# Kernel tuning notes

Hardware: AMD Instinct MI355X
Metric: run time of the kernel (lower is better)

Reference implementation:

```python
import jax, jax.numpy as jnp
import numpy as np

IN_CH, OUT_CH, K, STRIDE, PAD, NUM_POINTS = 16, 32, 3, 1, 1, 3
NUM_INPUTS = IN_CH * K * K  # 144
BATCH, H, W = 8, 32, 32


def setup_inputs() -> dict:
    key = jax.random.key(0)
    k1, k2, k3 = jax.random.split(key, 3)
    x = jax.random.normal(k1, (BATCH, IN_CH, H, W), dtype=jnp.float32)
    # sorted breakpoint positions per (input, output) pair in [-1, 1]
    base = jnp.linspace(-1.0, 1.0, NUM_POINTS, dtype=jnp.float32)
    jitter = 0.2 * (jax.random.uniform(k2, (NUM_INPUTS, OUT_CH, NUM_POINTS), dtype=jnp.float32) - 0.5) / NUM_POINTS
    positions = jnp.sort(base[None, None, :] + jitter, axis=-1)  # (I, O, P), sorted
    values = 0.1 * jax.random.normal(k3, (NUM_INPUTS, OUT_CH, NUM_POINTS), dtype=jnp.float32)
    return {"x": x, "positions": positions, "values": values}


def _gather_pt(table, idx):
    # table: (I, O, P), idx: (N, I, O) -> (N, I, O)
    return jnp.take_along_axis(table[None], idx[..., None], axis=-1)[..., 0]


def _piecewise(patches, positions, values):
    # patches: (N, I); positions/values: (I, O, P)
    P = positions.shape[-1]
    # bucket index: number of breakpoints <= x, clipped to a valid segment
    cmp = patches[:, :, None, None] >= positions[None]       # (N, I, O, P)
    idx = jnp.clip(cmp.sum(axis=-1) - 1, 0, P - 2)           # (N, I, O)
    pl = _gather_pt(positions, idx)
    pr = _gather_pt(positions, idx + 1)
    vl = _gather_pt(values, idx)
    vr = _gather_pt(values, idx + 1)
    t = (patches[:, :, None] - pl) / (pr - pl)               # (N, I, O)
    y = vl + t * (vr - vl)                                   # per-pair piecewise-linear value
    return y.sum(axis=1)                                     # (N, O): sum over input dims


def reference(x, positions, values):
    B, C, Hi, Wi = x.shape
    Ho = (Hi + 2 * PAD - K) // STRIDE + 1
    Wo = (Wi + 2 * PAD - K) // STRIDE + 1
    # im2col / unfold: (B, C*K*K, Ho, Wo) with (c, kh, kw) feature ordering like torch unfold
    patches = jax.lax.conv_general_dilated_patches(
        x, (K, K), (STRIDE, STRIDE), ((PAD, PAD), (PAD, PAD)))
    patches = patches.reshape(B, NUM_INPUTS, Ho * Wo).transpose(0, 2, 1).reshape(-1, NUM_INPUTS)
    out = _piecewise(patches, positions, values)             # (B*Ho*Wo, O)
    out = out.reshape(B, Ho * Wo, OUT_CH).transpose(0, 2, 1)
    return out.reshape(B, OUT_CH, Ho, Wo)
```

## Files before the change

### kernel.cpp

```cpp
#include <hip/hip_runtime.h>

#define IN_CH 16
#define OUT_CH 32
#define NUM_INPUTS 144
#define H_ 32
#define W_ 32

typedef __attribute__((ext_vector_type(2))) float f32x2;
typedef __attribute__((ext_vector_type(4))) float f32x4;

__global__ __launch_bounds__(512, 4) void apc_fused(
        const float* __restrict__ x,
        const float* __restrict__ pos,
        const float* __restrict__ val,
        float* __restrict__ out) {
    __shared__ f32x4 ltA[NUM_INPUTS * 16];
    __shared__ f32x2 ltD[NUM_INPUTS * 16];
    __shared__ float lx[IN_CH * 4 * 16];
    __shared__ f32x2 bpart[512];
    __shared__ f32x2 B0f[16];

    int tid  = threadIdx.x;
    int bx   = blockIdx.x;
    int b    = bx >> 6;
    int t64  = bx & 63;
    int row0 = (t64 >> 2) * 2;
    int col0 = (t64 & 3) * 8;

    #pragma unroll
    for (int it = 0; it < 2; ++it) {
        int s  = tid + it * 512;
        int c  = s >> 6;
        int rr = (s >> 4) & 3;
        int cl = s & 15;
        int gr = row0 + rr - 1;
        int gc = col0 + cl - 1;
        float v = 0.f;
        if (cl < 10 && (unsigned)gr < (unsigned)H_ && (unsigned)gc < (unsigned)W_)
            v = x[((b * IN_CH + c) * H_ + gr) * W_ + gc];
        lx[s] = v;
    }

    {
        int opb = tid & 15;
        int ib  = tid >> 4;
        f32x2 bs = {0.f, 0.f};
        #pragma unroll
        for (int k = 0; k < 5; ++k) {
            int i = ib + 32 * k;
            if (i < NUM_INPUTS) {
                const float* pp = pos + i * 96 + opb * 6;
                const float* vv = val + i * 96 + opb * 6;
                float q0a = pp[0], q1a = pp[1], q2a = pp[2];
                float q0b = pp[3], q1b = pp[4], q2b = pp[5];
                float w0a = vv[0], w1a = vv[1], w2a = vv[2];
                float w0b = vv[3], w1b = vv[4], w2b = vv[5];
                float s0a = (w1a - w0a) * __builtin_amdgcn_rcpf(q1a - q0a);
                float s1a = (w2a - w1a) * __builtin_amdgcn_rcpf(q2a - q1a);
                float s0b = (w1b - w0b) * __builtin_amdgcn_rcpf(q1b - q0b);
                float s1b = (w2b - w1b) * __builtin_amdgcn_rcpf(q2b - q1b);
                ltA[i * 16 + opb] = (f32x4){q1a, q1b, s0a, s0b};
                ltD[i * 16 + opb] = (f32x2){s1a - s0a, s1b - s0b};
                bs.x += w0a - s0a * q0a;
                bs.y += w0b - s0b * q0b;
            }
        }
        bpart[tid] = bs;
    }
    __syncthreads();

    if (tid < 16) {
        f32x2 s = {0.f, 0.f};
        #pragma unroll
        for (int g2 = 0; g2 < 32; ++g2) s += bpart[g2 * 16 + tid];
        B0f[tid] = s;
    }

    int wid  = tid >> 6;
    int lane = tid & 63;
    int sg   = lane >> 4;
    int op   = lane & 15;
    int r0   = sg >> 1;
    int cb   = (sg & 1) * 4;
    int c0   = wid * 2;

    f32x2 aacc[4], hacc[4];
    const f32x2 zz = {0.f, 0.f};
    #pragma unroll
    for (int j = 0; j < 4; ++j) { aacc[j] = zz; hacc[j] = zz; }

    const float* lxb = lx + (c0 * 4 + r0) * 16 + cb;
    const f32x4* Ab  = ltA + c0 * 144 + op;
    const f32x2* Db  = ltD + c0 * 144 + op;

    #pragma unroll
    for (int dc = 0; dc < 2; ++dc) {
        float w[3][6];
        #pragma unroll
        for (int dr = 0; dr < 3; ++dr) {
            f32x4 u = *(const f32x4*)(lxb + (dc * 4 + dr) * 16);
            f32x2 v = *(const f32x2*)(lxb + (dc * 4 + dr) * 16 + 4);
            w[dr][0] = u.x; w[dr][1] = u.y; w[dr][2] = u.z; w[dr][3] = u.w;
            w[dr][4] = v.x; w[dr][5] = v.y;
        }
        #pragma unroll
        for (int kh = 0; kh < 3; ++kh) {
            #pragma unroll
            for (int kw = 0; kw < 3; ++kw) {
                int ti = (dc * 9 + kh * 3 + kw) * 16;
                f32x4 A = Ab[ti];
                f32x2 D = Db[ti];
                f32x2 P = {A.x, A.y};
                f32x2 M = {A.z, A.w};
                #pragma unroll
                for (int j = 0; j < 4; ++j) {
                    f32x2 q = {w[kh][kw + j], w[kh][kw + j]};
                    aacc[j] = __builtin_elementwise_fma(M, q, aacc[j]);
                    hacc[j] = __builtin_elementwise_fma(
                        D, __builtin_elementwise_max(q - P, zz), hacc[j]);
                }
            }
        }
    }

    __syncthreads();
    {
        f32x2 s0 = aacc[0] + hacc[0], s1 = aacc[1] + hacc[1];
        f32x2 s2 = aacc[2] + hacc[2], s3 = aacc[3] + hacc[3];
        int rb = (wid * 64 + lane) * 2;
        ltA[rb + 0] = (f32x4){s0.x, s0.y, s1.x, s1.y};
        ltA[rb + 1] = (f32x4){s2.x, s2.y, s3.x, s3.y};
    }
    __syncthreads();

    if (tid < 256) {
        const f32x2* red = (const f32x2*)ltA;
        int opx = tid >> 4;
        int p   = tid & 15;
        int rr  = p >> 3;
        int cl  = p & 7;
        int sgx = rr * 2 + (cl >> 2);
        int j   = cl & 3;
        int base = (sgx * 16 + opx) * 4 + j;
        f32x2 s = B0f[opx];
        #pragma unroll
        for (int wv = 0; wv < 8; ++wv) s += red[wv * 256 + base];
        int oidx = ((b * OUT_CH + 2 * opx) * H_ + (row0 + rr)) * W_ + (col0 + cl);
        out[oidx]            = s.x;
        out[oidx + H_ * W_]  = s.y;
    }
}

extern "C" void kernel_launch(void* const* d_in, const int* in_sizes, int n_in,
                              void* d_out, int out_size, void* d_ws, size_t ws_size,
                              hipStream_t stream) {
    const float* x   = (const float*)d_in[0];
    const float* pos = (const float*)d_in[1];
    const float* val = (const float*)d_in[2];

    apc_fused<<<dim3(512), dim3(512), 0, stream>>>(x, pos, val, (float*)d_out);
}
```

Baseline: 63.74 us.

## Precompute piecewise-linear tables once in a separate kernel via workspace

```diff
diff --git a/kernel.cpp b/kernel.cpp
--- a/kernel.cpp
+++ b/kernel.cpp
@@ -5,19 +5,66 @@
 #define NUM_INPUTS 144
 #define H_ 32
 #define W_ 32
+#define NTAB 2304
 
 typedef __attribute__((ext_vector_type(2))) float f32x2;
 typedef __attribute__((ext_vector_type(4))) float f32x4;
 
+#define WS_TD 9216
+#define WS_B0 13824
+
+__global__ __launch_bounds__(256, 4) void apc_tables(
+        const float* __restrict__ pos,
+        const float* __restrict__ val,
+        float* __restrict__ ws) {
+    __shared__ f32x2 bpart[256];
+    f32x4* tAg = (f32x4*)ws;
+    f32x2* tDg = (f32x2*)(ws + WS_TD);
+    f32x2* B0p = (f32x2*)(ws + WS_B0);
+
+    int tid = threadIdx.x;
+    int e   = blockIdx.x * 256 + tid;
+    int i   = e >> 4;
+    int op  = e & 15;
+
+    const float* pp = pos + i * 96 + op * 6;
+    const float* vv = val + i * 96 + op * 6;
+    f32x2 pu0 = *(const f32x2*)(pp);
+    f32x2 pu1 = *(const f32x2*)(pp + 2);
+    f32x2 pu2 = *(const f32x2*)(pp + 4);
+    f32x2 vu0 = *(const f32x2*)(vv);
+    f32x2 vu1 = *(const f32x2*)(vv + 2);
+    f32x2 vu2 = *(const f32x2*)(vv + 4);
+    float q0a = pu0.x, q1a = pu0.y, q2a = pu1.x;
+    float q0b = pu1.y, q1b = pu2.x, q2b = pu2.y;
+    float w0a = vu0.x, w1a = vu0.y, w2a = vu1.x;
+    float w0b = vu1.y, w1b = vu2.x, w2b = vu2.y;
+
+    float s0a = (w1a - w0a) * __builtin_amdgcn_rcpf(q1a - q0a);
+    float s1a = (w2a - w1a) * __builtin_amdgcn_rcpf(q2a - q1a);
+    float s0b = (w1b - w0b) * __builtin_amdgcn_rcpf(q1b - q0b);
+    float s1b = (w2b - w1b) * __builtin_amdgcn_rcpf(q2b - q1b);
+
+    tAg[e] = (f32x4){q1a, q1b, s0a, s0b};
+    tDg[e] = (f32x2){s1a - s0a, s1b - s0b};
+
+    bpart[tid] = (f32x2){w0a - s0a * q0a, w0b - s0b * q0b};
+    __syncthreads();
+    if (tid < 16) {
+        f32x2 s = {0.f, 0.f};
+        #pragma unroll
+        for (int g = 0; g < 16; ++g) s += bpart[g * 16 + tid];
+        B0p[blockIdx.x * 16 + tid] = s;
+    }
+}
+
 __global__ __launch_bounds__(512, 4) void apc_fused(
         const float* __restrict__ x,
-        const float* __restrict__ pos,
-        const float* __restrict__ val,
+        const float* __restrict__ ws,
         float* __restrict__ out) {
-    __shared__ f32x4 ltA[NUM_INPUTS * 16];
-    __shared__ f32x2 ltD[NUM_INPUTS * 16];
+    __shared__ f32x4 ltA[NTAB];
+    __shared__ f32x2 ltD[NTAB];
     __shared__ float lx[IN_CH * 4 * 16];
-    __shared__ f32x2 bpart[512];
     __shared__ f32x2 B0f[16];
 
     int tid  = threadIdx.x;
@@ -42,39 +89,25 @@
     }
 
     {
-        int opb = tid & 15;
-        int ib  = tid >> 4;
-        f32x2 bs = {0.f, 0.f};
+        const f32x4* tAg = (const f32x4*)ws;
+        const f32x2* tDg = (const f32x2*)(ws + WS_TD);
         #pragma unroll
-        for (int k = 0; k < 5; ++k) {
-            int i = ib + 32 * k;
-            if (i < NUM_INPUTS) {
-                const float* pp = pos + i * 96 + opb * 6;
-                const float* vv = val + i * 96 + opb * 6;
-                float q0a = pp[0], q1a = pp[1], q2a = pp[2];
-                float q0b = pp[3], q1b = pp[4], q2b = pp[5];
-                float w0a = vv[0], w1a = vv[1], w2a = vv[2];
-                float w0b = vv[3], w1b = vv[4], w2b = vv[5];
-                float s0a = (w1a - w0a) * __builtin_amdgcn_rcpf(q1a - q0a);
-                float s1a = (w2a - w1a) * __builtin_amdgcn_rcpf(q2a - q1a);
-                float s0b = (w1b - w0b) * __builtin_amdgcn_rcpf(q1b - q0b);
-                float s1b = (w2b - w1b) * __builtin_amdgcn_rcpf(q2b - q1b);
-                ltA[i * 16 + opb] = (f32x4){q1a, q1b, s0a, s0b};
-                ltD[i * 16 + opb] = (f32x2){s1a - s0a, s1b - s0b};
-                bs.x += w0a - s0a * q0a;
-                bs.y += w0b - s0b * q0b;
-            }
+        for (int it = 0; it < 4; ++it) {
+            int e = tid + it * 512;
+            ltA[e] = tAg[e];
+            ltD[e] = tDg[e];
         }
-        bpart[tid] = bs;
+        int e4 = tid + 2048;
+        if (e4 < NTAB) { ltA[e4] = tAg[e4]; ltD[e4] = tDg[e4]; }
+        if (tid < 16) {
+            const f32x2* B0p = (const f32x2*)(ws + WS_B0);
+            f32x2 s = {0.f, 0.f};
+            #pragma unroll
+            for (int g = 0; g < 9; ++g) s += B0p[g * 16 + tid];
+            B0f[tid] = s;
+        }
     }
     __syncthreads();
-
-    if (tid < 16) {
-        f32x2 s = {0.f, 0.f};
-        #pragma unroll
-        for (int g2 = 0; g2 < 32; ++g2) s += bpart[g2 * 16 + tid];
-        B0f[tid] = s;
-    }
 
     int wid  = tid >> 6;
     int lane = tid & 63;
@@ -157,6 +190,8 @@
     const float* x   = (const float*)d_in[0];
     const float* pos = (const float*)d_in[1];
     const float* val = (const float*)d_in[2];
+    float*       ws  = (float*)d_ws;
 
-    apc_fused<<<dim3(512), dim3(512), 0, stream>>>(x, pos, val, (float*)d_out);
+    apc_tables<<<dim3(9),   dim3(256), 0, stream>>>(pos, val, ws);
+    apc_fused <<<dim3(512), dim3(512), 0, stream>>>(x, ws, (float*)d_out);
 }
```

Measured after the change: 64.56 us. Within noise of the previous version (+1.3%).

## Precompute breakpoint tables in separate kernel and hold per-thread coefficients in registers

Applied to the files above, without the earlier changes.

```diff
diff --git a/kernel.cpp b/kernel.cpp
--- a/kernel.cpp
+++ b/kernel.cpp
@@ -5,20 +5,54 @@
 #define NUM_INPUTS 144
 #define H_ 32
 #define W_ 32
+#define NENT 4608
 
 typedef __attribute__((ext_vector_type(2))) float f32x2;
 typedef __attribute__((ext_vector_type(4))) float f32x4;
 
+#define WS_TD 9216
+#define WS_B0 13824
+
+__global__ __launch_bounds__(512) void apc_tables(
+        const float* __restrict__ pos,
+        const float* __restrict__ val,
+        float* __restrict__ ws) {
+    __shared__ float bpart[512];
+    f32x2* tPM = (f32x2*)ws;
+    float* tD  = ws + WS_TD;
+    float* B0p = ws + WS_B0;
+
+    int tid = threadIdx.x;
+    int e   = blockIdx.x * 512 + tid;
+    int i   = e >> 5;
+    int o   = e & 31;
+
+    const float* pp = pos + i * 96 + o * 3;
+    const float* vv = val + i * 96 + o * 3;
+    float q0 = pp[0], q1 = pp[1], q2 = pp[2];
+    float w0 = vv[0], w1 = vv[1], w2 = vv[2];
+    float s0 = (w1 - w0) * __builtin_amdgcn_rcpf(q1 - q0);
+    float s1 = (w2 - w1) * __builtin_amdgcn_rcpf(q2 - q1);
+
+    tPM[e] = (f32x2){q1, s0};
+    tD[e]  = s1 - s0;
+    bpart[tid] = w0 - s0 * q0;
+    __syncthreads();
+    if (tid < 32) {
+        float s = 0.f;
+        #pragma unroll
+        for (int g = 0; g < 16; ++g) s += bpart[g * 32 + tid];
+        B0p[blockIdx.x * 32 + tid] = s;
+    }
+}
+
 __global__ __launch_bounds__(512, 4) void apc_fused(
         const float* __restrict__ x,
-        const float* __restrict__ pos,
-        const float* __restrict__ val,
+        const float* __restrict__ ws,
         float* __restrict__ out) {
-    __shared__ f32x4 ltA[NUM_INPUTS * 16];
-    __shared__ f32x2 ltD[NUM_INPUTS * 16];
     __shared__ float lx[IN_CH * 4 * 16];
-    __shared__ f32x2 bpart[512];
-    __shared__ f32x2 B0f[16];
+    __shared__ float red[8 * 512];
+    __shared__ float B0f[32];
 
     int tid  = threadIdx.x;
     int bx   = blockIdx.x;
@@ -40,114 +74,84 @@
             v = x[((b * IN_CH + c) * H_ + gr) * W_ + gc];
         lx[s] = v;
     }
-
-    {
-        int opb = tid & 15;
-        int ib  = tid >> 4;
-        f32x2 bs = {0.f, 0.f};
+    if (tid < 32) {
+        const float* B0p = ws + WS_B0;
+        float s = 0.f;
         #pragma unroll
-        for (int k = 0; k < 5; ++k) {
-            int i = ib + 32 * k;
-            if (i < NUM_INPUTS) {
-                const float* pp = pos + i * 96 + opb * 6;
-                const float* vv = val + i * 96 + opb * 6;
-                float q0a = pp[0], q1a = pp[1], q2a = pp[2];
-                float q0b = pp[3], q1b = pp[4], q2b = pp[5];
-                float w0a = vv[0], w1a = vv[1], w2a = vv[2];
-                float w0b = vv[3], w1b = vv[4], w2b = vv[5];
-                float s0a = (w1a - w0a) * __builtin_amdgcn_rcpf(q1a - q0a);
-                float s1a = (w2a - w1a) * __builtin_amdgcn_rcpf(q2a - q1a);
-                float s0b = (w1b - w0b) * __builtin_amdgcn_rcpf(q1b - q0b);
-                float s1b = (w2b - w1b) * __builtin_amdgcn_rcpf(q2b - q1b);
-                ltA[i * 16 + opb] = (f32x4){q1a, q1b, s0a, s0b};
-                ltD[i * 16 + opb] = (f32x2){s1a - s0a, s1b - s0b};
-                bs.x += w0a - s0a * q0a;
-                bs.y += w0b - s0b * q0b;
-            }
-        }
-        bpart[tid] = bs;
-    }
-    __syncthreads();
-
-    if (tid < 16) {
-        f32x2 s = {0.f, 0.f};
-        #pragma unroll
-        for (int g2 = 0; g2 < 32; ++g2) s += bpart[g2 * 16 + tid];
+        for (int g = 0; g < 9; ++g) s += B0p[g * 32 + tid];
         B0f[tid] = s;
     }
 
     int wid  = tid >> 6;
     int lane = tid & 63;
-    int sg   = lane >> 4;
-    int op   = lane & 15;
-    int r0   = sg >> 1;
-    int cb   = (sg & 1) * 4;
+    int sg   = lane >> 5;
+    int o    = lane & 31;
     int c0   = wid * 2;
+    int i0   = c0 * 9;
 
-    f32x2 aacc[4], hacc[4];
-    const f32x2 zz = {0.f, 0.f};
+    const f32x2* tPM = (const f32x2*)ws;
+    const float* tD  = ws + WS_TD;
+    f32x2 tpm[18];
+    float td[18];
     #pragma unroll
-    for (int j = 0; j < 4; ++j) { aacc[j] = zz; hacc[j] = zz; }
+    for (int k = 0; k < 18; ++k) {
+        tpm[k] = tPM[(i0 + k) * 32 + o];
+        td[k]  = tD [(i0 + k) * 32 + o];
+    }
+    __syncthreads();
 
-    const float* lxb = lx + (c0 * 4 + r0) * 16 + cb;
-    const f32x4* Ab  = ltA + c0 * 144 + op;
-    const f32x2* Db  = ltD + c0 * 144 + op;
-
+    float res[8];
     #pragma unroll
-    for (int dc = 0; dc < 2; ++dc) {
-        float w[3][6];
+    for (int half = 0; half < 2; ++half) {
+        int cb = half * 4;
+        float acc[4]  = {0.f, 0.f, 0.f, 0.f};
+        float hacc[4] = {0.f, 0.f, 0.f, 0.f};
         #pragma unroll
-        for (int dr = 0; dr < 3; ++dr) {
-            f32x4 u = *(const f32x4*)(lxb + (dc * 4 + dr) * 16);
-            f32x2 v = *(const f32x2*)(lxb + (dc * 4 + dr) * 16 + 4);
-            w[dr][0] = u.x; w[dr][1] = u.y; w[dr][2] = u.z; w[dr][3] = u.w;
-            w[dr][4] = v.x; w[dr][5] = v.y;
-        }
-        #pragma unroll
-        for (int kh = 0; kh < 3; ++kh) {
+        for (int dc = 0; dc < 2; ++dc) {
+            const float* lw = lx + ((c0 + dc) * 4 + sg) * 16 + cb;
+            float wv[3][6];
             #pragma unroll
-            for (int kw = 0; kw < 3; ++kw) {
-                int ti = (dc * 9 + kh * 3 + kw) * 16;
-                f32x4 A = Ab[ti];
-                f32x2 D = Db[ti];
-                f32x2 P = {A.x, A.y};
-                f32x2 M = {A.z, A.w};
+            for (int dr = 0; dr < 3; ++dr) {
+                f32x4 u  = *(const f32x4*)(lw + dr * 16);
+                f32x2 v2 = *(const f32x2*)(lw + dr * 16 + 4);
+                wv[dr][0] = u.x;  wv[dr][1] = u.y; wv[dr][2] = u.z;
+                wv[dr][3] = u.w;  wv[dr][4] = v2.x; wv[dr][5] = v2.y;
+            }
+            #pragma unroll
+            for (int kh = 0; kh < 3; ++kh) {
                 #pragma unroll
-                for (int j = 0; j < 4; ++j) {
-                    f32x2 q = {w[kh][kw + j], w[kh][kw + j]};
-                    aacc[j] = __builtin_elementwise_fma(M, q, aacc[j]);
-                    hacc[j] = __builtin_elementwise_fma(
-                        D, __builtin_elementwise_max(q - P, zz), hacc[j]);
+                for (int kw = 0; kw < 3; ++kw) {
+                    int k = dc * 9 + kh * 3 + kw;
+                    float p1 = tpm[k].x, m0 = tpm[k].y, dm = td[k];
+                    #pragma unroll
+                    for (int j = 0; j < 4; ++j) {
+                        float xv = wv[kh][kw + j];
+                        acc[j]  = fmaf(m0, xv, acc[j]);
+                        hacc[j] = fmaf(dm, fmaxf(xv - p1, 0.f), hacc[j]);
+                    }
                 }
             }
         }
+        #pragma unroll
+        for (int j = 0; j < 4; ++j) res[half * 4 + j] = acc[j] + hacc[j];
     }
 
+    {
+        float* rw = red + wid * 512 + sg * 32;
+        #pragma unroll
+        for (int j = 0; j < 8; ++j)
+            rw[j * 64 + ((o + 4 * j) & 31)] = res[j];
+    }
     __syncthreads();
     {
-        f32x2 s0 = aacc[0] + hacc[0], s1 = aacc[1] + hacc[1];
-        f32x2 s2 = aacc[2] + hacc[2], s3 = aacc[3] + hacc[3];
-        int rb = (wid * 64 + lane) * 2;
-        ltA[rb + 0] = (f32x4){s0.x, s0.y, s1.x, s1.y};
-        ltA[rb + 1] = (f32x4){s2.x, s2.y, s3.x, s3.y};
-    }
-    __syncthreads();
-
-    if (tid < 256) {
-        const f32x2* red = (const f32x2*)ltA;
-        int opx = tid >> 4;
-        int p   = tid & 15;
-        int rr  = p >> 3;
-        int cl  = p & 7;
-        int sgx = rr * 2 + (cl >> 2);
-        int j   = cl & 3;
-        int base = (sgx * 16 + opx) * 4 + j;
-        f32x2 s = B0f[opx];
+        int j   = tid & 7;
+        int o2  = (tid >> 3) & 31;
+        int sg2 = tid >> 8;
+        int ra  = j * 64 + sg2 * 32 + ((o2 + 4 * j) & 31);
+        float s = B0f[o2];
         #pragma unroll
-        for (int wv = 0; wv < 8; ++wv) s += red[wv * 256 + base];
-        int oidx = ((b * OUT_CH + 2 * opx) * H_ + (row0 + rr)) * W_ + (col0 + cl);
-        out[oidx]            = s.x;
-        out[oidx + H_ * W_]  = s.y;
+        for (int wv2 = 0; wv2 < 8; ++wv2) s += red[wv2 * 512 + ra];
+        out[((b * OUT_CH + o2) * H_ + row0 + sg2) * W_ + col0 + j] = s;
     }
 }
 
@@ -157,6 +161,8 @@
     const float* x   = (const float*)d_in[0];
     const float* pos = (const float*)d_in[1];
     const float* val = (const float*)d_in[2];
+    float*       ws  = (float*)d_ws;
 
-    apc_fused<<<dim3(512), dim3(512), 0, stream>>>(x, pos, val, (float*)d_out);
+    apc_tables<<<dim3(9),   dim3(512), 0, stream>>>(pos, val, ws);
+    apc_fused <<<dim3(512), dim3(512), 0, stream>>>(x, ws, (float*)d_out);
 }
```

New measurement: 64.63 us. No clear change (+1.4%).
